# Kernel optimization log

Measured on AMD Instinct MI355X. Metric: run time of the kernel, lower is better.

The kernel has to match this reference:

```python
import jax, jax.numpy as jnp
import numpy as np

B, T, D, H = 2048, 200, 64, 64


def setup_inputs() -> dict:
    key = jax.random.key(0)
    ks = jax.random.split(key, 5)
    rnn_input = jax.random.normal(ks[0], (B, T, D), dtype=jnp.float32)
    sequence_length = jax.random.randint(ks[1], (B,), 0, T, dtype=jnp.int32)
    att_score = jax.random.uniform(ks[2], (B, T, 1), dtype=jnp.float32)
    # glorot-uniform-style init for kernels; TF VecAttGRUCell uses constant 1.0 gate bias
    s = np.float32(np.sqrt(6.0 / (D + H + 2 * H)))
    gate_kernel = jax.random.uniform(ks[3], (D + H, 2 * H), jnp.float32, -s, s)
    gate_bias = jnp.ones((2 * H,), jnp.float32)
    sc = np.float32(np.sqrt(6.0 / (D + H + H)))
    cand_kernel = jax.random.uniform(ks[4], (D + H, H), jnp.float32, -sc, sc)
    cand_bias = jnp.zeros((H,), jnp.float32)
    return dict(rnn_input=rnn_input, sequence_length=sequence_length,
                att_score=att_score, gate_kernel=gate_kernel, gate_bias=gate_bias,
                cand_kernel=cand_kernel, cand_bias=cand_bias)


def _augru(rnn_input, sequence_length, att_score, gate_kernel, gate_bias, cand_kernel, cand_bias):
    # rnn_input: [B,T,D], att_score: [B,T,1], sequence_length: [B]
    Bn, Tn, _ = rnn_input.shape
    Hn = cand_kernel.shape[1]
    x_t = jnp.swapaxes(rnn_input, 0, 1)   # [T,B,D]
    a_t = jnp.swapaxes(att_score, 0, 1)   # [T,B,1]
    t_idx = jnp.arange(Tn)
    h0 = jnp.zeros((Bn, Hn), rnn_input.dtype)

    def step(h, inp):
        x, a, t = inp
        gates = jax.nn.sigmoid(jnp.concatenate([x, h], axis=-1) @ gate_kernel + gate_bias)
        r, u = jnp.split(gates, 2, axis=-1)                       # [B,H] each
        c = jnp.tanh(jnp.concatenate([x, r * h], axis=-1) @ cand_kernel + cand_bias)
        u_hat = (1.0 - a) * u                                      # attention-modulated update gate
        new_h = u_hat * h + (1.0 - u_hat) * c
        valid = (t < sequence_length)[:, None]                     # dynamic_rnn semantics
        h_next = jnp.where(valid, new_h, h)                        # freeze state past seq len
        out = jnp.where(valid, new_h, jnp.zeros_like(new_h))       # zero outputs past seq len
        return h_next, out

    h_last, outs = jax.lax.scan(step, h0, (x_t, a_t, t_idx))
    return jnp.swapaxes(outs, 0, 1), h_last  # [B,T,H], [B,H]


def reference(rnn_input, sequence_length, att_score, gate_kernel, gate_bias, cand_kernel, cand_bias):
    outputs, _ = _augru(rnn_input, sequence_length, att_score,
                        gate_kernel, gate_bias, cand_kernel, cand_bias)
    return outputs  # return_sequence=True
```

## Files before the change

### kernel.cpp

```cpp
#include <hip/hip_runtime.h>

#define Tn 200
#define Dn 64
#define Hn 64
#define CC 16

typedef _Float16 half2v __attribute__((ext_vector_type(2)));
typedef _Float16 half8v __attribute__((ext_vector_type(8)));
typedef float    f32x4  __attribute__((ext_vector_type(4)));

__device__ __forceinline__ float fast_sigmoid(float v) {
    return __builtin_amdgcn_rcpf(1.0f + __expf(-v));
}
__device__ __forceinline__ float fast_tanh(float v) {
    return 1.0f - 2.0f * __builtin_amdgcn_rcpf(1.0f + __expf(2.0f * v));
}

__device__ __forceinline__ void cfence() {
    asm volatile("" ::: "memory");
}
__device__ __forceinline__ void wave_lds_fence() {
    asm volatile("s_waitcnt lgkmcnt(0)" ::: "memory");
}

__device__ __forceinline__ half8v cvt8(const float4 a, const float4 b) {
    return half8v{(_Float16)a.x, (_Float16)a.y, (_Float16)a.z, (_Float16)a.w,
                  (_Float16)b.x, (_Float16)b.y, (_Float16)b.z, (_Float16)b.w};
}

__global__ __launch_bounds__(256, 4)
void augru_proj_mfma(const float* __restrict__ x,
                     const int*   __restrict__ slen,
                     const float* __restrict__ gk,
                     const float* __restrict__ gb,
                     const float* __restrict__ ck,
                     const float* __restrict__ cb,
                     _Float16*    __restrict__ P,
                     int nrows, int nchunks)
{
    const int tid  = threadIdx.x;
    const int w    = tid >> 6;
    const int lane = tid & 63;
    const int lm   = lane & 15;
    const int kq   = lane >> 4;

    half8v bf[3][2];
    float  bias[3];
#pragma unroll
    for (int nt = 0; nt < 3; ++nt) {
        const int n = w * 48 + nt * 16 + lm;
#pragma unroll
        for (int kh = 0; kh < 2; ++kh) {
            const int kb = kh * 32 + kq * 8;
            half8v f;
#pragma unroll
            for (int e = 0; e < 8; ++e) {
                const int k = kb + e;
                const float v = (n < 128) ? gk[k * 128 + n]
                                          : ck[k * 64 + (n - 128)];
                f[e] = (_Float16)v;
            }
            bf[nt][kh] = f;
        }
        bias[nt] = (n < 128) ? gb[n] : cb[n - 128];
    }

    for (int chunk = blockIdx.x; chunk < nchunks; chunk += gridDim.x) {
        const int rb0 = chunk * 64;
#pragma unroll
        for (int sub = 0; sub < 4; ++sub) {
            const int rb = rb0 + sub * 16;

            const int rowv = rb + lm;
            const int bv   = rowv / Tn;
            const int tv   = rowv - bv * Tn;
            const bool v   = (rowv < nrows) && (tv < slen[bv]);
            if (__ballot(v) == 0ull) continue;

            const int rowA = min(rb + lm, nrows - 1);
            const float* xr = x + (size_t)rowA * Dn + kq * 8;
            const float4 q0 = *(const float4*)(xr);
            const float4 q1 = *(const float4*)(xr + 4);
            const float4 q2 = *(const float4*)(xr + 32);
            const float4 q3 = *(const float4*)(xr + 36);
            const half8v a0 = cvt8(q0, q1);
            const half8v a1 = cvt8(q2, q3);

            f32x4 acc[3];
#pragma unroll
            for (int nt = 0; nt < 3; ++nt) {
                f32x4 c = {bias[nt], bias[nt], bias[nt], bias[nt]};
                c = __builtin_amdgcn_mfma_f32_16x16x32_f16(a0, bf[nt][0], c, 0, 0, 0);
                c = __builtin_amdgcn_mfma_f32_16x16x32_f16(a1, bf[nt][1], c, 0, 0, 0);
                acc[nt] = c;
            }

#pragma unroll
            for (int r = 0; r < 4; ++r) {
                const int row = rb + kq * 4 + r;
                const int bb  = row / Tn;
                const int tt  = row - bb * Tn;
                if (row < nrows && tt < slen[bb]) {
                    _Float16* Pt = P + (size_t)row * 192 + w * 48 + lm;
                    Pt[0]  = (_Float16)acc[0][r];
                    Pt[16] = (_Float16)acc[1][r];
                    Pt[32] = (_Float16)acc[2][r];
                }
            }
        }
    }
}

__global__ __launch_bounds__(64, 2)
void augru_rec(const _Float16* __restrict__ P,
               const int*     __restrict__ slen,
               const float*   __restrict__ att,
               const float*   __restrict__ gk,
               const float*   __restrict__ ck,
               float*         __restrict__ out)
{
    const int b = blockIdx.x;
    const int j = threadIdx.x;

    __shared__ __align__(16) _Float16 s_h[Hn];
    __shared__ __align__(16) _Float16 s_rh[Hn];

    half2v wr[32], wu[32], wc[32];
#pragma unroll
    for (int m = 0; m < 32; ++m) {
        const int k = 64 + 2 * m;
        wr[m] = half2v{(_Float16)gk[(k + 0) * 128 + j],
                       (_Float16)gk[(k + 1) * 128 + j]};
        wu[m] = half2v{(_Float16)gk[(k + 0) * 128 + 64 + j],
                       (_Float16)gk[(k + 1) * 128 + 64 + j]};
        wc[m] = half2v{(_Float16)ck[(k + 0) * 64 + j],
                       (_Float16)ck[(k + 1) * 64 + j]};
    }

    const int len = slen[b];
    const _Float16* Prow = P   + (size_t)b * Tn * 192;
    const float*    arow = att + (size_t)b * Tn;
    float*          orow = out + (size_t)b * Tn * Hn;

    float h = 0.0f;

    _Float16 pr_n = (_Float16)0, pu_n = (_Float16)0, pc_n = (_Float16)0;
    float a_n = 0.0f;
    if (len > 0) {
        pr_n = Prow[j]; pu_n = Prow[64 + j]; pc_n = Prow[128 + j];
        a_n  = arow[0];
    }

    for (int t = 0; t < len; ++t) {
        const float pr = (float)pr_n;
        const float pu = (float)pu_n;
        const float pc = (float)pc_n;
        const float a  = a_n;
        const int tn = min(t + 1, len - 1);
        const _Float16* Pt = Prow + (size_t)tn * 192;
        pr_n = Pt[j]; pu_n = Pt[64 + j]; pc_n = Pt[128 + j];
        a_n  = arow[tn];

        s_h[j] = (_Float16)h;
        cfence();

        float r0 = pr, r1 = 0.f, u0 = pu, u1 = 0.f;
        const half8v* hv = (const half8v*)s_h;
#pragma unroll
        for (int m8 = 0; m8 < 8; ++m8) {
            const half8v v = hv[m8];
            const half2v p0 = __builtin_shufflevector(v, v, 0, 1);
            const half2v p1 = __builtin_shufflevector(v, v, 2, 3);
            const half2v p2 = __builtin_shufflevector(v, v, 4, 5);
            const half2v p3 = __builtin_shufflevector(v, v, 6, 7);
            const int m = m8 * 4;
            r0 = __builtin_amdgcn_fdot2(p0, wr[m + 0], r0, false);
            r1 = __builtin_amdgcn_fdot2(p1, wr[m + 1], r1, false);
            r0 = __builtin_amdgcn_fdot2(p2, wr[m + 2], r0, false);
            r1 = __builtin_amdgcn_fdot2(p3, wr[m + 3], r1, false);
            u0 = __builtin_amdgcn_fdot2(p0, wu[m + 0], u0, false);
            u1 = __builtin_amdgcn_fdot2(p1, wu[m + 1], u1, false);
            u0 = __builtin_amdgcn_fdot2(p2, wu[m + 2], u0, false);
            u1 = __builtin_amdgcn_fdot2(p3, wu[m + 3], u1, false);
        }
        const float rg = fast_sigmoid(r0 + r1);
        const float ug = fast_sigmoid(u0 + u1);

        s_rh[j] = (_Float16)(rg * h);
        cfence();

        float c0 = pc, c1 = 0.f;
        const half8v* rv = (const half8v*)s_rh;
#pragma unroll
        for (int m8 = 0; m8 < 8; ++m8) {
            const half8v v = rv[m8];
            const half2v p0 = __builtin_shufflevector(v, v, 0, 1);
            const half2v p1 = __builtin_shufflevector(v, v, 2, 3);
            const half2v p2 = __builtin_shufflevector(v, v, 4, 5);
            const half2v p3 = __builtin_shufflevector(v, v, 6, 7);
            const int m = m8 * 4;
            c0 = __builtin_amdgcn_fdot2(p0, wc[m + 0], c0, false);
            c1 = __builtin_amdgcn_fdot2(p1, wc[m + 1], c1, false);
            c0 = __builtin_amdgcn_fdot2(p2, wc[m + 2], c0, false);
            c1 = __builtin_amdgcn_fdot2(p3, wc[m + 3], c1, false);
        }
        const float cg = fast_tanh(c0 + c1);

        const float uh = (1.0f - a) * ug;
        h = uh * h + (1.0f - uh) * cg;
        orow[t * Hn + j] = h;
        cfence();
    }

    float4 z;
    z.x = z.y = z.z = z.w = 0.0f;
    float* tail = orow + (size_t)len * Hn;
    const int total = (Tn - len) * Hn;
    for (int i = j * 4; i < total; i += 64 * 4) {
        *(float4*)(tail + i) = z;
    }
}

__global__ __launch_bounds__(128, 2)
void augru_fused_fb(const float* __restrict__ x, const int* __restrict__ slen,
                    const float* __restrict__ att, const float* __restrict__ gk,
                    const float* __restrict__ gb, const float* __restrict__ ck,
                    const float* __restrict__ cb, float* __restrict__ out)
{
    const int b    = blockIdx.x;
    const int tid  = threadIdx.x;
    const int wave = tid >> 6;
    const int j    = tid & 63;

    __shared__ float s_P[2][CC][3][Hn];
    __shared__ __align__(16) _Float16 s_h[Hn];
    __shared__ __align__(16) _Float16 s_rh[Hn];

    const int len     = slen[b];
    const int nchunks = (len + CC - 1) / CC;
    const float* xrow = x   + (size_t)b * Tn * Dn;
    const float* arow = att + (size_t)b * Tn;
    float*       orow = out + (size_t)b * Tn * Hn;

    if (wave == 0) {
        half2v wr[32], wu[32], wc[32];
#pragma unroll
        for (int m = 0; m < 32; ++m) {
            const int k = 2 * m;
            wr[m] = half2v{(_Float16)gk[(k + 0) * 128 + j], (_Float16)gk[(k + 1) * 128 + j]};
            wu[m] = half2v{(_Float16)gk[(k + 0) * 128 + 64 + j], (_Float16)gk[(k + 1) * 128 + 64 + j]};
            wc[m] = half2v{(_Float16)ck[(k + 0) * 64 + j], (_Float16)ck[(k + 1) * 64 + j]};
        }
        const float br = gb[j], bu = gb[64 + j], bc = cb[j];
        for (int c = 0; c < nchunks; ++c) {
            const int t0 = c * CC, tend = min(len, t0 + CC);
            for (int t = t0; t < tend; ++t) {
                const float4* xv = (const float4*)(xrow + t * Dn);
                float r0 = br, r1 = 0.f, u0 = bu, u1 = 0.f, c0 = bc, c1 = 0.f;
#pragma unroll
                for (int kk = 0; kk < 16; ++kk) {
                    const float4 q = xv[kk];
                    const half2v p0 = half2v{(_Float16)q.x, (_Float16)q.y};
                    const half2v p1 = half2v{(_Float16)q.z, (_Float16)q.w};
                    const int m = 2 * kk;
                    r0 = __builtin_amdgcn_fdot2(p0, wr[m], r0, false);
                    r1 = __builtin_amdgcn_fdot2(p1, wr[m + 1], r1, false);
                    u0 = __builtin_amdgcn_fdot2(p0, wu[m], u0, false);
                    u1 = __builtin_amdgcn_fdot2(p1, wu[m + 1], u1, false);
                    c0 = __builtin_amdgcn_fdot2(p0, wc[m], c0, false);
                    c1 = __builtin_amdgcn_fdot2(p1, wc[m + 1], c1, false);
                }
                const int lt = t - t0;
                s_P[c & 1][lt][0][j] = r0 + r1;
                s_P[c & 1][lt][1][j] = u0 + u1;
                s_P[c & 1][lt][2][j] = c0 + c1;
            }
            __syncthreads();
        }
    } else {
        half2v wr[32], wu[32], wc[32];
#pragma unroll
        for (int m = 0; m < 32; ++m) {
            const int k = 64 + 2 * m;
            wr[m] = half2v{(_Float16)gk[(k + 0) * 128 + j], (_Float16)gk[(k + 1) * 128 + j]};
            wu[m] = half2v{(_Float16)gk[(k + 0) * 128 + 64 + j], (_Float16)gk[(k + 1) * 128 + 64 + j]};
            wc[m] = half2v{(_Float16)ck[(k + 0) * 64 + j], (_Float16)ck[(k + 1) * 64 + j]};
        }
        float h = 0.0f;
        for (int c = 0; c < nchunks; ++c) {
            __syncthreads();
            const int t0 = c * CC, tend = min(len, t0 + CC);
            for (int t = t0; t < tend; ++t) {
                const int lt = t - t0;
                const float pr = s_P[c & 1][lt][0][j];
                const float pu = s_P[c & 1][lt][1][j];
                const float pc = s_P[c & 1][lt][2][j];
                const float a  = arow[t];
                s_h[j] = (_Float16)h;
                wave_lds_fence();
                float r0 = pr, r1 = 0.f, u0 = pu, u1 = 0.f;
                const half8v* hv = (const half8v*)s_h;
#pragma unroll
                for (int m8 = 0; m8 < 8; ++m8) {
                    const half8v v = hv[m8];
                    const half2v p0 = __builtin_shufflevector(v, v, 0, 1);
                    const half2v p1 = __builtin_shufflevector(v, v, 2, 3);
                    const half2v p2 = __builtin_shufflevector(v, v, 4, 5);
                    const half2v p3 = __builtin_shufflevector(v, v, 6, 7);
                    const int m = m8 * 4;
                    r0 = __builtin_amdgcn_fdot2(p0, wr[m + 0], r0, false);
                    r1 = __builtin_amdgcn_fdot2(p1, wr[m + 1], r1, false);
                    r0 = __builtin_amdgcn_fdot2(p2, wr[m + 2], r0, false);
                    r1 = __builtin_amdgcn_fdot2(p3, wr[m + 3], r1, false);
                    u0 = __builtin_amdgcn_fdot2(p0, wu[m + 0], u0, false);
                    u1 = __builtin_amdgcn_fdot2(p1, wu[m + 1], u1, false);
                    u0 = __builtin_amdgcn_fdot2(p2, wu[m + 2], u0, false);
                    u1 = __builtin_amdgcn_fdot2(p3, wu[m + 3], u1, false);
                }
                const float rg = fast_sigmoid(r0 + r1);
                const float ug = fast_sigmoid(u0 + u1);
                s_rh[j] = (_Float16)(rg * h);
                wave_lds_fence();
                float c0 = pc, c1 = 0.f;
                const half8v* rv = (const half8v*)s_rh;
#pragma unroll
                for (int m8 = 0; m8 < 8; ++m8) {
                    const half8v v = rv[m8];
                    const half2v p0 = __builtin_shufflevector(v, v, 0, 1);
                    const half2v p1 = __builtin_shufflevector(v, v, 2, 3);
                    const half2v p2 = __builtin_shufflevector(v, v, 4, 5);
                    const half2v p3 = __builtin_shufflevector(v, v, 6, 7);
                    const int m = m8 * 4;
                    c0 = __builtin_amdgcn_fdot2(p0, wc[m + 0], c0, false);
                    c1 = __builtin_amdgcn_fdot2(p1, wc[m + 1], c1, false);
                    c0 = __builtin_amdgcn_fdot2(p2, wc[m + 2], c0, false);
                    c1 = __builtin_amdgcn_fdot2(p3, wc[m + 3], c1, false);
                }
                const float cg = fast_tanh(c0 + c1);
                const float uh = (1.0f - a) * ug;
                h = uh * h + (1.0f - uh) * cg;
                orow[t * Hn + j] = h;
                wave_lds_fence();
            }
        }
    }
    float4 z; z.x = z.y = z.z = z.w = 0.0f;
    float* tail = orow + len * Hn;
    const int total = (Tn - len) * Hn;
    for (int i = tid * 4; i < total; i += 128 * 4) *(float4*)(tail + i) = z;
}

extern "C" void kernel_launch(void* const* d_in, const int* in_sizes, int n_in,
                              void* d_out, int out_size, void* d_ws, size_t ws_size,
                              hipStream_t stream) {
    const float* x    = (const float*)d_in[0];
    const int*   slen = (const int*)  d_in[1];
    const float* att  = (const float*)d_in[2];
    const float* gk   = (const float*)d_in[3];
    const float* gb   = (const float*)d_in[4];
    const float* ck   = (const float*)d_in[5];
    const float* cb   = (const float*)d_in[6];
    float* out = (float*)d_out;

    const int B = in_sizes[1];
    const size_t needP = (size_t)B * Tn * 192 * sizeof(_Float16);

    if (ws_size >= needP) {
        _Float16* P = (_Float16*)d_ws;
        const int nrows   = B * Tn;
        const int nchunks = (nrows + 63) / 64;
        const int grid    = nchunks < 1024 ? nchunks : 1024;
        augru_proj_mfma<<<grid, 256, 0, stream>>>(x, slen, gk, gb, ck, cb, P,
                                                  nrows, nchunks);
        augru_rec<<<B, 64, 0, stream>>>(P, slen, att, gk, ck, out);
    } else {
        augru_fused_fb<<<B, 128, 0, stream>>>(x, slen, att, gk, gb, ck, cb, out);
    }
}
```

Before: 358.5 us.

## Restructure projection kernel to single-wave blocks with LDS-staged coalesced stores

The projection kernel now runs one 64-lane wave per block covering all 192 output columns (12 MFMA tiles), instead of four waves each covering 48 columns. Results are staged in shared memory and written to the workspace as 16-byte vector stores per row, replacing scattered 2-byte stores. This targets poor store coalescing and the per-row validity checks. The cost is more weight registers per lane. It also drops the per-row validity masking on stores, so P rows past the sequence length now get written too. It assumes nrows is a multiple of 16 and uses only a compiler fence, not a barrier, between the LDS writes and reads.

After: 350.6 us. 2.2% less time.

```diff
diff --git a/kernel.cpp b/kernel.cpp
--- a/kernel.cpp
+++ b/kernel.cpp
@@ -8,6 +8,7 @@
 typedef _Float16 half2v __attribute__((ext_vector_type(2)));
 typedef _Float16 half8v __attribute__((ext_vector_type(8)));
 typedef float    f32x4  __attribute__((ext_vector_type(4)));
+typedef unsigned int uint;
 
 __device__ __forceinline__ float fast_sigmoid(float v) {
     return __builtin_amdgcn_rcpf(1.0f + __expf(-v));
@@ -15,7 +16,6 @@
 __device__ __forceinline__ float fast_tanh(float v) {
     return 1.0f - 2.0f * __builtin_amdgcn_rcpf(1.0f + __expf(2.0f * v));
 }
-
 __device__ __forceinline__ void cfence() {
     asm volatile("" ::: "memory");
 }
@@ -28,7 +28,7 @@
                   (_Float16)b.x, (_Float16)b.y, (_Float16)b.z, (_Float16)b.w};
 }
 
-__global__ __launch_bounds__(256, 4)
+__global__ __launch_bounds__(64, 1)
 void augru_proj_mfma(const float* __restrict__ x,
                      const int*   __restrict__ slen,
                      const float* __restrict__ gk,
@@ -36,78 +36,69 @@
                      const float* __restrict__ ck,
                      const float* __restrict__ cb,
                      _Float16*    __restrict__ P,
-                     int nrows, int nchunks)
+                     int nsub)
 {
-    const int tid  = threadIdx.x;
-    const int w    = tid >> 6;
-    const int lane = tid & 63;
+    const int lane = threadIdx.x;
     const int lm   = lane & 15;
     const int kq   = lane >> 4;
 
-    half8v bf[3][2];
-    float  bias[3];
-#pragma unroll
-    for (int nt = 0; nt < 3; ++nt) {
-        const int n = w * 48 + nt * 16 + lm;
+    __shared__ __align__(16) _Float16 sbuf[16][200];
+
+    half8v bf[12][2];
+    float  bias[12];
+#pragma unroll
+    for (int nt = 0; nt < 12; ++nt) {
+        const int n = nt * 16 + lm;
 #pragma unroll
         for (int kh = 0; kh < 2; ++kh) {
-            const int kb = kh * 32 + kq * 8;
             half8v f;
 #pragma unroll
             for (int e = 0; e < 8; ++e) {
-                const int k = kb + e;
-                const float v = (n < 128) ? gk[k * 128 + n]
-                                          : ck[k * 64 + (n - 128)];
-                f[e] = (_Float16)v;
+                const int k = kh * 32 + kq * 8 + e;
+                f[e] = (_Float16)((n < 128) ? gk[k * 128 + n]
+                                            : ck[k * 64 + (n - 128)]);
             }
             bf[nt][kh] = f;
         }
         bias[nt] = (n < 128) ? gb[n] : cb[n - 128];
     }
 
-    for (int chunk = blockIdx.x; chunk < nchunks; chunk += gridDim.x) {
-        const int rb0 = chunk * 64;
-#pragma unroll
-        for (int sub = 0; sub < 4; ++sub) {
-            const int rb = rb0 + sub * 16;
-
-            const int rowv = rb + lm;
-            const int bv   = rowv / Tn;
-            const int tv   = rowv - bv * Tn;
-            const bool v   = (rowv < nrows) && (tv < slen[bv]);
-            if (__ballot(v) == 0ull) continue;
-
-            const int rowA = min(rb + lm, nrows - 1);
-            const float* xr = x + (size_t)rowA * Dn + kq * 8;
-            const float4 q0 = *(const float4*)(xr);
-            const float4 q1 = *(const float4*)(xr + 4);
-            const float4 q2 = *(const float4*)(xr + 32);
-            const float4 q3 = *(const float4*)(xr + 36);
-            const half8v a0 = cvt8(q0, q1);
-            const half8v a1 = cvt8(q2, q3);
-
-            f32x4 acc[3];
-#pragma unroll
-            for (int nt = 0; nt < 3; ++nt) {
-                f32x4 c = {bias[nt], bias[nt], bias[nt], bias[nt]};
-                c = __builtin_amdgcn_mfma_f32_16x16x32_f16(a0, bf[nt][0], c, 0, 0, 0);
-                c = __builtin_amdgcn_mfma_f32_16x16x32_f16(a1, bf[nt][1], c, 0, 0, 0);
-                acc[nt] = c;
-            }
-
-#pragma unroll
-            for (int r = 0; r < 4; ++r) {
-                const int row = rb + kq * 4 + r;
-                const int bb  = row / Tn;
-                const int tt  = row - bb * Tn;
-                if (row < nrows && tt < slen[bb]) {
-                    _Float16* Pt = P + (size_t)row * 192 + w * 48 + lm;
-                    Pt[0]  = (_Float16)acc[0][r];
-                    Pt[16] = (_Float16)acc[1][r];
-                    Pt[32] = (_Float16)acc[2][r];
-                }
-            }
-        }
+    for (int s = blockIdx.x; s < nsub; s += gridDim.x) {
+        const int rb = s * 16;
+
+        const int rowv = rb + lm;
+        const int bv   = rowv / Tn;
+        const int tv   = rowv - bv * Tn;
+        if (__ballot(tv < slen[bv]) == 0ull) continue;
+
+        const float* xr = x + (size_t)rowv * Dn + kq * 8;
+        const float4 q0 = *(const float4*)(xr);
+        const float4 q1 = *(const float4*)(xr + 4);
+        const float4 q2 = *(const float4*)(xr + 32);
+        const float4 q3 = *(const float4*)(xr + 36);
+        const half8v a0 = cvt8(q0, q1);
+        const half8v a1 = cvt8(q2, q3);
+
+#pragma unroll
+        for (int nt = 0; nt < 12; ++nt) {
+            f32x4 c = {bias[nt], bias[nt], bias[nt], bias[nt]};
+            c = __builtin_amdgcn_mfma_f32_16x16x32_f16(a0, bf[nt][0], c, 0, 0, 0);
+            c = __builtin_amdgcn_mfma_f32_16x16x32_f16(a1, bf[nt][1], c, 0, 0, 0);
+#pragma unroll
+            for (int r = 0; r < 4; ++r)
+                sbuf[kq * 4 + r][nt * 16 + lm] = (_Float16)c[r];
+        }
+        cfence();
+
+#pragma unroll
+        for (int i = 0; i < 6; ++i) {
+            const int idx = i * 64 + lane;
+            const int row = idx / 24;
+            const int c16 = idx % 24;
+            const uint4 v = *(const uint4*)&sbuf[row][c16 * 8];
+            *(uint4*)(P + (size_t)(rb + row) * 192 + c16 * 8) = v;
+        }
+        cfence();
     }
 }
 
@@ -367,11 +358,10 @@
 
     if (ws_size >= needP) {
         _Float16* P = (_Float16*)d_ws;
-        const int nrows   = B * Tn;
-        const int nchunks = (nrows + 63) / 64;
-        const int grid    = nchunks < 1024 ? nchunks : 1024;
-        augru_proj_mfma<<<grid, 256, 0, stream>>>(x, slen, gk, gb, ck, cb, P,
-                                                  nrows, nchunks);
+        const int nrows = B * Tn;
+        const int nsub  = nrows / 16;
+        const int grid  = nsub < 8192 ? nsub : 8192;
+        augru_proj_mfma<<<grid, 64, 0, stream>>>(x, slen, gk, gb, ck, cb, P, nsub);
         augru_rec<<<B, 64, 0, stream>>>(P, slen, att, gk, ck, out);
     } else {
         augru_fused_fb<<<B, 128, 0, stream>>>(x, slen, att, gk, gb, ck, cb, out);
```
